# Kernel tuning notes

Hardware: AMD Instinct MI355X
Metric: run time of the kernel (lower is better)

Reference implementation:

```python
import jax, jax.numpy as jnp
import numpy as np
import math

N, E, D, H, L = 50000, 800000, 256, 8, 8
DK = D // H
DFF = 4 * D


def _layernorm(h, g, b, eps=1e-5):
    m = jnp.mean(h, axis=-1, keepdims=True)
    v = jnp.mean((h - m) ** 2, axis=-1, keepdims=True)
    return (h - m) * jax.lax.rsqrt(v + eps) * g + b


def setup_inputs() -> dict:
    key = jax.random.key(0)
    ks = jax.random.split(key, 16)
    s = 1.0 / math.sqrt(D)
    x = jax.random.normal(ks[0], (N, D), dtype=jnp.float32)
    # every node gets >=1 in-edge so z > 0 everywhere (as in real connected graphs)
    edge_src = jax.random.randint(ks[1], (E,), 0, N, dtype=jnp.int32)
    edge_dst = jnp.concatenate([
        jnp.arange(N, dtype=jnp.int32),
        jax.random.randint(ks[2], (E - N,), 0, N, dtype=jnp.int32),
    ])
    return {
        "x": x,
        "edge_src": edge_src,
        "edge_dst": edge_dst,
        "Wq": jax.random.normal(ks[3], (L, D, D), dtype=jnp.float32) * s,
        "bq": jnp.zeros((L, D), dtype=jnp.float32),
        "Wk": jax.random.normal(ks[4], (L, D, D), dtype=jnp.float32) * s,
        "Wv": jax.random.normal(ks[5], (L, D, D), dtype=jnp.float32) * s,
        "Wo": jax.random.normal(ks[6], (L, D, D), dtype=jnp.float32) * s,
        "bo": jnp.zeros((L, D), dtype=jnp.float32),
        "ln1_g": jnp.ones((L, D), dtype=jnp.float32),
        "ln1_b": jnp.zeros((L, D), dtype=jnp.float32),
        "W1": jax.random.normal(ks[7], (L, D, DFF), dtype=jnp.float32) * s,
        "b1": jnp.zeros((L, DFF), dtype=jnp.float32),
        "W2": jax.random.normal(ks[8], (L, DFF, D), dtype=jnp.float32) * (1.0 / math.sqrt(DFF)),
        "b2": jnp.zeros((L, D), dtype=jnp.float32),
        "ln2_g": jnp.ones((L, D), dtype=jnp.float32),
        "ln2_b": jnp.zeros((L, D), dtype=jnp.float32),
    }


def _layer(x, src, dst, Wq, bq, Wk, Wv, Wo, bo, g1, b1n, W1, b1, W2, b2, g2, b2n):
    n = x.shape[0]
    q = (x @ Wq + bq).reshape(n, H, DK)
    k = (x @ Wk).reshape(n, H, DK)
    v = (x @ Wv).reshape(n, H, DK)
    # edge score: src_dot_dst('k','q') -> [E, H]
    score = jnp.einsum('ehd,ehd->eh', k[src], q[dst])
    # scaled_exp: exp(clamp(score / sqrt(d_k), -5, 5))
    score = jnp.exp(jnp.clip(score / math.sqrt(DK), -5.0, 5.0))
    # u_mul_e + sum aggregation -> wv [N, H, DK]; copy_edge + sum -> z [N, H]
    msg = v[src] * score[:, :, None]
    wv = jax.ops.segment_sum(msg, dst, num_segments=n)
    z = jax.ops.segment_sum(score, dst, num_segments=n)
    o = (wv / z[:, :, None]).reshape(n, D)
    h = _layernorm(x + o @ Wo + bo, g1, b1n)
    # FFN with residual + layernorm
    ff = jax.nn.relu(h @ W1 + b1) @ W2 + b2
    return _layernorm(h + ff, g2, b2n)


def reference(x, edge_src, edge_dst, Wq, bq, Wk, Wv, Wo, bo, ln1_g, ln1_b,
              W1, b1, W2, b2, ln2_g, ln2_b):
    for i in range(L):
        x = _layer(x, edge_src, edge_dst, Wq[i], bq[i], Wk[i], Wv[i], Wo[i],
                   bo[i], ln1_g[i], ln1_b[i], W1[i], b1[i], W2[i], b2[i],
                   ln2_g[i], ln2_b[i])
    return x
```

## Files before the change

kernel.cpp:

```cpp
#include <hip/hip_runtime.h>
#include <cstdint>
#include <cstddef>

#define D 256
#define H 8
#define DFF 1024

typedef short s16x8 __attribute__((ext_vector_type(8)));
typedef float f32x4 __attribute__((ext_vector_type(4)));

static inline int cdiv(int a, int b) { return (a + b - 1) / b; }

__device__ inline uint16_t f2bf(float x) {
    unsigned u = __float_as_uint(x);
    u += 0x7FFFu + ((u >> 16) & 1u);
    return (uint16_t)(u >> 16);
}
__device__ inline float bf2f(uint16_t h) {
    return __uint_as_float(((unsigned)h) << 16);
}

__device__ inline void gload_lds16(const void* g, void* l) {
    __builtin_amdgcn_global_load_lds(
        (const __attribute__((address_space(1))) void*)g,
        (__attribute__((address_space(3))) void*)l, 16, 0, 0);
}

__device__ inline void vmcnt0() { asm volatile("s_waitcnt vmcnt(0)" ::: "memory"); }
__device__ inline void vmcnt4() { asm volatile("s_waitcnt vmcnt(4)" ::: "memory"); }
__device__ inline void vmcnt5() { asm volatile("s_waitcnt vmcnt(5)" ::: "memory"); }
__device__ inline void vmcnt6() { asm volatile("s_waitcnt vmcnt(6)" ::: "memory"); }
__device__ inline void lgkm0()  { asm volatile("s_waitcnt lgkmcnt(0)" ::: "memory"); }
#define SB0() __builtin_amdgcn_sched_barrier(0)
#define BARF() do { SB0(); __builtin_amdgcn_s_barrier(); SB0(); } while (0)

__global__ __launch_bounds__(256) void zero_int_kernel(int* __restrict__ p, int count)
{
    int i = blockIdx.x * blockDim.x + threadIdx.x;
    if (i < count) p[i] = 0;
}

__global__ __launch_bounds__(256) void count_deg_kernel(
    const int* __restrict__ edst, int* __restrict__ deg, int E)
{
    int e = blockIdx.x * blockDim.x + threadIdx.x;
    if (e < E) atomicAdd(&deg[edst[e]], 1);
}

__global__ __launch_bounds__(256) void block_sum_kernel(
    const int* __restrict__ deg, int* __restrict__ bsum, int N)
{
    int t = threadIdx.x;
    int gid = blockIdx.x * 256 + t;
    int val = (gid < N) ? deg[gid] : 0;
    #pragma unroll
    for (int o = 1; o < 64; o <<= 1) val += __shfl_xor(val, o);
    __shared__ int r[4];
    if ((t & 63) == 0) r[t >> 6] = val;
    __syncthreads();
    if (t == 0) bsum[blockIdx.x] = r[0] + r[1] + r[2] + r[3];
}

__global__ __launch_bounds__(256) void scan_bsum_kernel(int* __restrict__ bsum, int nb)
{
    __shared__ int tmp[256];
    int t = threadIdx.x;
    int val = (t < nb) ? bsum[t] : 0;
    tmp[t] = val;
    __syncthreads();
    for (int off = 1; off < 256; off <<= 1) {
        int add = (t >= off) ? tmp[t - off] : 0;
        __syncthreads();
        tmp[t] += add;
        __syncthreads();
    }
    if (t < nb) bsum[t] = tmp[t] - val;
}

__global__ __launch_bounds__(256) void scan_write_kernel(
    const int* __restrict__ deg, const int* __restrict__ bsum,
    int* __restrict__ rowptr, int* __restrict__ cursor, int N)
{
    __shared__ int tmp[256];
    int t = threadIdx.x;
    int gid = blockIdx.x * 256 + t;
    int val = (gid < N) ? deg[gid] : 0;
    tmp[t] = val;
    __syncthreads();
    for (int off = 1; off < 256; off <<= 1) {
        int add = (t >= off) ? tmp[t - off] : 0;
        __syncthreads();
        tmp[t] += add;
        __syncthreads();
    }
    int excl = tmp[t] - val + bsum[blockIdx.x];
    if (gid < N) { rowptr[gid] = excl; cursor[gid] = excl; }
    if (gid == N - 1) rowptr[N] = excl + val;
}

__global__ __launch_bounds__(256) void fill_csr_kernel(
    const int* __restrict__ esrc, const int* __restrict__ edst,
    int* __restrict__ cursor, int* __restrict__ csr_src, int E)
{
    int e = blockIdx.x * blockDim.x + threadIdx.x;
    if (e < E) {
        int pos = atomicAdd(&cursor[edst[e]], 1);
        csr_src[pos] = esrc[e];
    }
}

__global__ __launch_bounds__(256) void transpose_cast_kernel(
    const float* __restrict__ in, uint16_t* __restrict__ out,
    int R, int C, size_t inLS, size_t outLS)
{
    __shared__ float t[32][33];
    in  += blockIdx.z * inLS;
    out += blockIdx.z * outLS;
    int c0 = blockIdx.x * 32, r0 = blockIdx.y * 32;
    int tx = threadIdx.x, ty = threadIdx.y;
    #pragma unroll
    for (int i = 0; i < 4; ++i)
        t[ty + i * 8][tx] = in[(size_t)(r0 + ty + i * 8) * C + c0 + tx];
    __syncthreads();
    #pragma unroll
    for (int i = 0; i < 4; ++i)
        out[(size_t)(c0 + ty + i * 8) * R + r0 + tx] = f2bf(t[tx][ty + i * 8]);
}

__global__ __launch_bounds__(256) void cast_f32_bf16_kernel(
    const float* __restrict__ in, uint16_t* __restrict__ out, int n4)
{
    int i = blockIdx.x * blockDim.x + threadIdx.x;
    if (i >= n4) return;
    float4 f = ((const float4*)in)[i];
    uint16_t o0 = f2bf(f.x), o1 = f2bf(f.y), o2 = f2bf(f.z), o3 = f2bf(f.w);
    uint2 pk;
    pk.x = (unsigned)o0 | ((unsigned)o1 << 16);
    pk.y = (unsigned)o2 | ((unsigned)o3 << 16);
    ((uint2*)out)[i] = pk;
}

__global__ __launch_bounds__(256) void build_qkv_bias_kernel(
    const float* __restrict__ bq, float* __restrict__ qb, int total)
{
    int i = blockIdx.x * blockDim.x + threadIdx.x;
    if (i >= total) return;
    int l = i / 768, c = i - l * 768;
    qb[i] = (c < 256) ? bq[l * 256 + c] : 0.f;
}

__global__ __launch_bounds__(256) void gemm_bf16_kernel(
    const uint16_t* __restrict__ A, int lda, int M, int K,
    const uint16_t* __restrict__ BT, int Nc,
    const float* __restrict__ bias,
    uint16_t* __restrict__ Cb, int relu)
{
    __shared__ __align__(16) uint16_t As[2][128 * 32];
    __shared__ __align__(16) uint16_t Bs[2][128 * 32];

    const int tid  = threadIdx.x;
    const int lane = tid & 63;
    const int w    = tid >> 6;
    const int wr   = w >> 1, wc = w & 1;
    const int quad = lane >> 4;
    const int l15  = lane & 15;

    const int nwg = gridDim.x * gridDim.y;
    const int lin = blockIdx.y * gridDim.x + blockIdx.x;
    const int xcd = lin & 7, idx = lin >> 3;
    const int q8 = nwg >> 3, r8 = nwg & 7;
    const int lin2 = (xcd < r8 ? xcd * (q8 + 1) : r8 * (q8 + 1) + (xcd - r8) * q8) + idx;
    const int mt = lin2 % gridDim.x;
    const int nt = lin2 / gridDim.x;

    const int m0 = mt * 128;
    const int n0 = nt * 128;

    f32x4 acc[4][4] = {};

    const int jbase = w * 2;
    const int srow  = lane >> 2;
    const int skc   = (lane & 3) * 8;

    auto stage = [&](int b, int k0) {
        #pragma unroll
        for (int jj = 0; jj < 2; ++jj) {
            int j = jbase + jj;
            int r = j * 16 + srow;
            int gr = m0 + r; if (gr > M - 1) gr = M - 1;
            gload_lds16(A  + (size_t)gr * lda + k0 + skc, &As[b][j * 512]);
            gload_lds16(BT + (size_t)(n0 + r) * K + k0 + skc, &Bs[b][j * 512]);
        }
    };

    const int nsteps = K >> 5;
    stage(0, 0);
    for (int s = 0; s < nsteps; ++s) {
        if (s + 1 < nsteps) { stage((s + 1) & 1, (s + 1) << 5); vmcnt4(); }
        else vmcnt0();
        BARF();
        const int b = s & 1;
        s16x8 af[4], bf[4];
        #pragma unroll
        for (int t = 0; t < 4; ++t) {
            af[t] = *(const s16x8*)&As[b][(wr * 64 + t * 16 + l15) * 32 + quad * 8];
            bf[t] = *(const s16x8*)&Bs[b][(wc * 64 + t * 16 + l15) * 32 + quad * 8];
        }
        #pragma unroll
        for (int i = 0; i < 4; ++i)
            #pragma unroll
            for (int jt = 0; jt < 4; ++jt)
                acc[i][jt] = __builtin_amdgcn_mfma_f32_16x16x32_bf16(
                    af[i], bf[jt], acc[i][jt], 0, 0, 0);
        BARF();
    }

    float bv[4];
    #pragma unroll
    for (int jt = 0; jt < 4; ++jt)
        bv[jt] = bias ? bias[n0 + wc * 64 + jt * 16 + l15] : 0.f;

    #pragma unroll
    for (int i = 0; i < 4; ++i) {
        #pragma unroll
        for (int r = 0; r < 4; ++r) {
            int m = m0 + wr * 64 + i * 16 + quad * 4 + r;
            if (m >= M) continue;
            #pragma unroll
            for (int jt = 0; jt < 4; ++jt) {
                int n = n0 + wc * 64 + jt * 16 + l15;
                float val = acc[i][jt][r] + bv[jt];
                if (relu) val = fmaxf(val, 0.f);
                Cb[(size_t)m * Nc + n] = f2bf(val);
            }
        }
    }
}

__global__ __launch_bounds__(256) void gemm_ln_kernel(
    const uint16_t* __restrict__ A, int lda, int M, int K,
    const uint16_t* __restrict__ BT,
    const float* __restrict__ bias,
    const float* __restrict__ resid,
    const float* __restrict__ g, const float* __restrict__ b,
    float* __restrict__ Cf, uint16_t* __restrict__ Cb)
{
    __shared__ __align__(16) uint16_t As[2][64 * 32];
    __shared__ __align__(16) uint16_t Bs[2][256 * 32];
    __shared__ float sS[64][4];
    __shared__ float sQ[64][4];

    const int tid  = threadIdx.x;
    const int lane = tid & 63;
    const int w    = tid >> 6;
    const int quad = lane >> 4;
    const int l15  = lane & 15;

    const int m0 = blockIdx.x * 64;

    f32x4 acc[4][4] = {};

    auto stage = [&](int bb, int k0) {
        {
            int r = tid >> 2, kc = (tid & 3) * 8;
            int gr = m0 + r; if (gr > M - 1) gr = M - 1;
            gload_lds16(A + (size_t)gr * lda + k0 + kc, &As[bb][tid * 8]);
        }
        #pragma unroll
        for (int i = 0; i < 4; ++i) {
            int slot = i * 256 + tid;
            int n = slot >> 2, kc = (slot & 3) * 8;
            gload_lds16(BT + (size_t)n * K + k0 + kc, &Bs[bb][slot * 8]);
        }
    };

    const int nsteps = K >> 5;
    stage(0, 0);
    for (int s = 0; s < nsteps; ++s) {
        if (s + 1 < nsteps) { stage((s + 1) & 1, (s + 1) << 5); vmcnt5(); }
        else vmcnt0();
        BARF();
        const int bb = s & 1;
        s16x8 af[4], bf[4];
        #pragma unroll
        for (int t = 0; t < 4; ++t) {
            af[t] = *(const s16x8*)&As[bb][(t * 16 + l15) * 32 + quad * 8];
            bf[t] = *(const s16x8*)&Bs[bb][(w * 64 + t * 16 + l15) * 32 + quad * 8];
        }
        #pragma unroll
        for (int i = 0; i < 4; ++i)
            #pragma unroll
            for (int jt = 0; jt < 4; ++jt)
                acc[i][jt] = __builtin_amdgcn_mfma_f32_16x16x32_bf16(
                    af[i], bf[jt], acc[i][jt], 0, 0, 0);
        BARF();
    }

    float bv[4], gv[4], bbv[4];
    #pragma unroll
    for (int jt = 0; jt < 4; ++jt) {
        int n = w * 64 + jt * 16 + l15;
        bv[jt]  = bias[n];
        gv[jt]  = g[n];
        bbv[jt] = b[n];
    }

    #pragma unroll
    for (int i = 0; i < 4; ++i) {
        #pragma unroll
        for (int r = 0; r < 4; ++r) {
            int ml = i * 16 + quad * 4 + r;
            int m  = m0 + ml;
            bool valid = (m < M);
            float s = 0.f, s2 = 0.f;
            #pragma unroll
            for (int jt = 0; jt < 4; ++jt) {
                int n = w * 64 + jt * 16 + l15;
                float val = acc[i][jt][r] + bv[jt];
                if (valid) val += resid[(size_t)m * 256 + n];
                acc[i][jt][r] = val;
                s += val;
                s2 += val * val;
            }
            #pragma unroll
            for (int o = 1; o < 16; o <<= 1) {
                s  += __shfl_xor(s, o);
                s2 += __shfl_xor(s2, o);
            }
            if (l15 == 0) { sS[ml][w] = s; sQ[ml][w] = s2; }
        }
    }
    __syncthreads();

    #pragma unroll
    for (int i = 0; i < 4; ++i) {
        #pragma unroll
        for (int r = 0; r < 4; ++r) {
            int ml = i * 16 + quad * 4 + r;
            int m  = m0 + ml;
            if (m >= M) continue;
            float s  = sS[ml][0] + sS[ml][1] + sS[ml][2] + sS[ml][3];
            float s2 = sQ[ml][0] + sQ[ml][1] + sQ[ml][2] + sQ[ml][3];
            float mean = s * (1.f / 256.f);
            float var  = s2 * (1.f / 256.f) - mean * mean;
            float rstd = rsqrtf(var + 1e-5f);
            #pragma unroll
            for (int jt = 0; jt < 4; ++jt) {
                int n = w * 64 + jt * 16 + l15;
                float out = (acc[i][jt][r] - mean) * rstd * gv[jt] + bbv[jt];
                Cf[(size_t)m * 256 + n] = out;
                if (Cb) Cb[(size_t)m * 256 + n] = f2bf(out);
            }
        }
    }
}

__global__ __launch_bounds__(256) void ffn_fused_kernel(
    const uint16_t* __restrict__ A,
    int M,
    const uint16_t* __restrict__ BT1,
    const float* __restrict__ b1,
    const uint16_t* __restrict__ BT2,
    const float* __restrict__ b2,
    const float* __restrict__ resid,
    const float* __restrict__ g, const float* __restrict__ b,
    float* __restrict__ Cf, uint16_t* __restrict__ Cb)
{
    __shared__ __align__(16) uint16_t U[3][8192];
    __shared__ __align__(16) uint16_t Ts[4][64][32];

    const int tid  = threadIdx.x;
    const int lane = tid & 63;
    const int w    = tid >> 6;
    const int quad = lane >> 4;
    const int l15  = lane & 15;
    const int m0   = blockIdx.x * 64;

    f32x4 acc2[4][4] = {};

    auto issue = [&](int q) {
        if (q >= 96) return;
        const int slot = q % 3;
        const int qc = q / 12;
        const int r  = q - qc * 12;
        if (r < 8) {
            const int k0 = r << 5;
            {
                int rr = tid >> 2, kc = (tid & 3) * 8;
                int gr = m0 + rr; if (gr > M - 1) gr = M - 1;
                gload_lds16(A + (size_t)gr * 256 + k0 + kc, &U[slot][tid * 8]);
            }
            #pragma unroll
            for (int i = 0; i < 2; ++i) {
                int s2 = i * 256 + tid;
                int n = s2 >> 2, kc = (s2 & 3) * 8;
                gload_lds16(BT1 + (size_t)(qc * 128 + n) * 256 + k0 + kc,
                            &U[slot][2048 + s2 * 8]);
            }
        } else {
            const int ts = r - 8;
            #pragma unroll
            for (int i = 0; i < 4; ++i) {
                int s2 = i * 256 + tid;
                int n = s2 >> 2, kc = (s2 & 3) * 8;
                gload_lds16(BT2 + (size_t)n * 1024 + qc * 128 + ts * 32 + kc,
                            &U[slot][s2 * 8]);
            }
        }
    };

    issue(0);
    issue(1);

    for (int c = 0; c < 8; ++c) {
        f32x4 acc1[4][2] = {};
        const int pbase = c * 12;

        for (int ks = 0; ks < 8; ++ks) {
            const int p = pbase + ks;
            issue(p + 2);
            vmcnt6();
            BARF();
            const uint16_t* Us = U[p % 3];
            s16x8 af[4], bf1[2];
            #pragma unroll
            for (int t = 0; t < 4; ++t)
                af[t] = *(const s16x8*)&Us[(t * 16 + l15) * 32 + quad * 8];
            #pragma unroll
            for (int jt = 0; jt < 2; ++jt)
                bf1[jt] = *(const s16x8*)&Us[2048 + (w * 32 + jt * 16 + l15) * 32 + quad * 8];
            #pragma unroll
            for (int i = 0; i < 4; ++i)
                #pragma unroll
                for (int jt = 0; jt < 2; ++jt)
                    acc1[i][jt] = __builtin_amdgcn_mfma_f32_16x16x32_bf16(
                        af[i], bf1[jt], acc1[i][jt], 0, 0, 0);
            BARF();
        }

        float bv1[2];
        #pragma unroll
        for (int jt = 0; jt < 2; ++jt)
            bv1[jt] = b1[c * 128 + w * 32 + jt * 16 + l15];
        {
            uint16_t* tsw = &Ts[w][0][0];
            #pragma unroll
            for (int i = 0; i < 4; ++i)
                #pragma unroll
                for (int r = 0; r < 4; ++r) {
                    int ml = i * 16 + quad * 4 + r;
                    int sw = ((ml >> 1) & 3) << 3;
                    #pragma unroll
                    for (int jt = 0; jt < 2; ++jt) {
                        float val = acc1[i][jt][r] + bv1[jt];
                        val = fmaxf(val, 0.f);
                        tsw[(ml * 32 + jt * 16 + l15) ^ sw] = f2bf(val);
                    }
                }
        }
        lgkm0();
        BARF();

        for (int ts = 0; ts < 4; ++ts) {
            const int p = pbase + 8 + ts;
            issue(p + 2);
            if (c == 7 && ts == 2) vmcnt4();
            else if (c == 7 && ts == 3) vmcnt0();
            else vmcnt6();
            BARF();
            const uint16_t* Us = U[p % 3];
            const uint16_t* tsr = &Ts[ts][0][0];
            s16x8 af2[4], bf2[4];
            #pragma unroll
            for (int i = 0; i < 4; ++i) {
                int row = i * 16 + l15;
                af2[i] = *(const s16x8*)&tsr[(row * 32 + quad * 8) ^ (((row >> 1) & 3) << 3)];
            }
            #pragma unroll
            for (int jt = 0; jt < 4; ++jt)
                bf2[jt] = *(const s16x8*)&Us[(w * 64 + jt * 16 + l15) * 32 + quad * 8];
            #pragma unroll
            for (int i = 0; i < 4; ++i)
                #pragma unroll
                for (int jt = 0; jt < 4; ++jt)
                    acc2[i][jt] = __builtin_amdgcn_mfma_f32_16x16x32_bf16(
                        af2[i], bf2[jt], acc2[i][jt], 0, 0, 0);
            BARF();
        }
    }

    float* sS = (float*)&U[0][0];
    float* sQ = (float*)&U[0][512];

    float bv[4], gv[4], bbv[4];
    #pragma unroll
    for (int jt = 0; jt < 4; ++jt) {
        int n = w * 64 + jt * 16 + l15;
        bv[jt]  = b2[n];
        gv[jt]  = g[n];
        bbv[jt] = b[n];
    }

    #pragma unroll
    for (int i = 0; i < 4; ++i) {
        #pragma unroll
        for (int r = 0; r < 4; ++r) {
            int ml = i * 16 + quad * 4 + r;
            int m  = m0 + ml;
            bool valid = (m < M);
            float s = 0.f, s2 = 0.f;
            #pragma unroll
            for (int jt = 0; jt < 4; ++jt) {
                float val = acc2[i][jt][r] + bv[jt];
                if (valid) val += resid[(size_t)m * 256 + w * 64 + jt * 16 + l15];
                acc2[i][jt][r] = val;
                s += val;
                s2 += val * val;
            }
            #pragma unroll
            for (int o = 1; o < 16; o <<= 1) {
                s  += __shfl_xor(s, o);
                s2 += __shfl_xor(s2, o);
            }
            if (l15 == 0) { sS[ml * 4 + w] = s; sQ[ml * 4 + w] = s2; }
        }
    }
    __syncthreads();

    #pragma unroll
    for (int i = 0; i < 4; ++i) {
        #pragma unroll
        for (int r = 0; r < 4; ++r) {
            int ml = i * 16 + quad * 4 + r;
            int m  = m0 + ml;
            if (m >= M) continue;
            float s  = sS[ml * 4 + 0] + sS[ml * 4 + 1] + sS[ml * 4 + 2] + sS[ml * 4 + 3];
            float s2 = sQ[ml * 4 + 0] + sQ[ml * 4 + 1] + sQ[ml * 4 + 2] + sQ[ml * 4 + 3];
            float mean = s * (1.f / 256.f);
            float var  = s2 * (1.f / 256.f) - mean * mean;
            float rstd = rsqrtf(var + 1e-5f);
            #pragma unroll
            for (int jt = 0; jt < 4; ++jt) {
                int n = w * 64 + jt * 16 + l15;
                float out = (acc2[i][jt][r] - mean) * rstd * gv[jt] + bbv[jt];
                Cf[(size_t)m * 256 + n] = out;
                if (Cb) Cb[(size_t)m * 256 + n] = f2bf(out);
            }
        }
    }
}

__global__ __launch_bounds__(256) void node_attn_kernel(
    uint16_t* __restrict__ qkv,
    const int* __restrict__ rowptr, const int* __restrict__ csr_src, int N)
{
    int node = (blockIdx.x * blockDim.x + threadIdx.x) >> 6;
    int lane = threadIdx.x & 63;
    if (node >= N) return;

    uint16_t* qp = qkv + (size_t)node * 768 + lane * 4;
    uint2 qu = *(const uint2*)qp;
    float q0 = bf2f((uint16_t)(qu.x & 0xFFFF)), q1 = bf2f((uint16_t)(qu.x >> 16));
    float q2 = bf2f((uint16_t)(qu.y & 0xFFFF)), q3 = bf2f((uint16_t)(qu.y >> 16));

    float a0 = 0.f, a1 = 0.f, a2 = 0.f, a3 = 0.f, zacc = 0.f;
    const float inv_sqrt_dk = 0.17677669529663687f;

    int beg = rowptr[node], end = rowptr[node + 1];
    int i = beg;
    for (; i + 1 < end; i += 2) {
        int s0 = csr_src[i], s1 = csr_src[i + 1];
        const uint16_t* b0 = qkv + (size_t)s0 * 768;
        const uint16_t* b1 = qkv + (size_t)s1 * 768;
        uint2 ku0 = *(const uint2*)(b0 + 256 + lane * 4);
        uint2 ku1 = *(const uint2*)(b1 + 256 + lane * 4);
        uint2 vu0 = *(const uint2*)(b0 + 512 + lane * 4);
        uint2 vu1 = *(const uint2*)(b1 + 512 + lane * 4);

        float p0 = bf2f((uint16_t)(ku0.x & 0xFFFF)) * q0
                 + bf2f((uint16_t)(ku0.x >> 16))   * q1
                 + bf2f((uint16_t)(ku0.y & 0xFFFF)) * q2
                 + bf2f((uint16_t)(ku0.y >> 16))   * q3;
        float p1 = bf2f((uint16_t)(ku1.x & 0xFFFF)) * q0
                 + bf2f((uint16_t)(ku1.x >> 16))   * q1
                 + bf2f((uint16_t)(ku1.y & 0xFFFF)) * q2
                 + bf2f((uint16_t)(ku1.y >> 16))   * q3;
        p0 += __shfl_xor(p0, 1); p1 += __shfl_xor(p1, 1);
        p0 += __shfl_xor(p0, 2); p1 += __shfl_xor(p1, 2);
        p0 += __shfl_xor(p0, 4); p1 += __shfl_xor(p1, 4);
        float sc0 = __expf(fminf(fmaxf(p0 * inv_sqrt_dk, -5.f), 5.f));
        float sc1 = __expf(fminf(fmaxf(p1 * inv_sqrt_dk, -5.f), 5.f));

        a0 += bf2f((uint16_t)(vu0.x & 0xFFFF)) * sc0;
        a1 += bf2f((uint16_t)(vu0.x >> 16))   * sc0;
        a2 += bf2f((uint16_t)(vu0.y & 0xFFFF)) * sc0;
        a3 += bf2f((uint16_t)(vu0.y >> 16))   * sc0;
        zacc += sc0;
        a0 += bf2f((uint16_t)(vu1.x & 0xFFFF)) * sc1;
        a1 += bf2f((uint16_t)(vu1.x >> 16))   * sc1;
        a2 += bf2f((uint16_t)(vu1.y & 0xFFFF)) * sc1;
        a3 += bf2f((uint16_t)(vu1.y >> 16))   * sc1;
        zacc += sc1;
    }
    if (i < end) {
        int s = csr_src[i];
        const uint16_t* base = qkv + (size_t)s * 768;
        uint2 ku = *(const uint2*)(base + 256 + lane * 4);
        float p = bf2f((uint16_t)(ku.x & 0xFFFF)) * q0
                + bf2f((uint16_t)(ku.x >> 16))   * q1
                + bf2f((uint16_t)(ku.y & 0xFFFF)) * q2
                + bf2f((uint16_t)(ku.y >> 16))   * q3;
        p += __shfl_xor(p, 1);
        p += __shfl_xor(p, 2);
        p += __shfl_xor(p, 4);
        float sc = __expf(fminf(fmaxf(p * inv_sqrt_dk, -5.f), 5.f));
        uint2 vu = *(const uint2*)(base + 512 + lane * 4);
        a0 += bf2f((uint16_t)(vu.x & 0xFFFF)) * sc;
        a1 += bf2f((uint16_t)(vu.x >> 16))   * sc;
        a2 += bf2f((uint16_t)(vu.y & 0xFFFF)) * sc;
        a3 += bf2f((uint16_t)(vu.y >> 16))   * sc;
        zacc += sc;
    }
    float inv = 1.f / zacc;
    uint2 pk;
    pk.x = (unsigned)f2bf(a0 * inv) | ((unsigned)f2bf(a1 * inv) << 16);
    pk.y = (unsigned)f2bf(a2 * inv) | ((unsigned)f2bf(a3 * inv) << 16);
    *(uint2*)qp = pk;
}

extern "C" void kernel_launch(void* const* d_in, const int* in_sizes, int n_in,
                              void* d_out, int out_size, void* d_ws, size_t ws_size,
                              hipStream_t stream)
{
    const float* x0   = (const float*)d_in[0];
    const int* esrc   = (const int*)d_in[1];
    const int* edst   = (const int*)d_in[2];
    const float* Wq   = (const float*)d_in[3];
    const float* bq   = (const float*)d_in[4];
    const float* Wk   = (const float*)d_in[5];
    const float* Wv   = (const float*)d_in[6];
    const float* Wo   = (const float*)d_in[7];
    const float* bo   = (const float*)d_in[8];
    const float* ln1g = (const float*)d_in[9];
    const float* ln1b = (const float*)d_in[10];
    const float* W1   = (const float*)d_in[11];
    const float* b1   = (const float*)d_in[12];
    const float* W2   = (const float*)d_in[13];
    const float* b2   = (const float*)d_in[14];
    const float* ln2g = (const float*)d_in[15];
    const float* ln2b = (const float*)d_in[16];

    const int N = in_sizes[0] / D;
    const int E = in_sizes[1];
    const int L = in_sizes[3] / (D * D);
    const size_t ND = (size_t)N * D;

    char* p = (char*)d_ws;
    float* bufX = (float*)p;         p += ND * 4;
    uint16_t* xb  = (uint16_t*)p;    p += ND * 2;
    uint16_t* qkv = (uint16_t*)p;    p += (size_t)N * 768 * 2;
    uint16_t* hb  = (uint16_t*)p;    p += ND * 2;
    uint16_t* BTqkv = (uint16_t*)p;  p += (size_t)L * 768 * 256 * 2;
    uint16_t* BTo   = (uint16_t*)p;  p += (size_t)L * 256 * 256 * 2;
    uint16_t* BT1   = (uint16_t*)p;  p += (size_t)L * 1024 * 256 * 2;
    uint16_t* BT2   = (uint16_t*)p;  p += (size_t)L * 256 * 1024 * 2;
    float* qbias    = (float*)p;     p += (size_t)L * 768 * 4;
    int* rowptr  = (int*)p;          p += (size_t)(N + 1) * 4;
    int* cursor  = (int*)p;          p += (size_t)N * 4;
    int* deg     = cursor;
    int* csr_src = (int*)p;          p += (size_t)E * 4;
    int* bsum    = (int*)p;

    const int nb = cdiv(N, 256);
    dim3 blk(256);
    int edgeBlocks = cdiv(E, 256);
    int nodeBlocks = cdiv(N, 4);

    dim3 tb(32, 8);
    transpose_cast_kernel<<<dim3(8, 8, L), tb, 0, stream>>>(Wq, BTqkv, 256, 256, (size_t)65536, (size_t)768 * 256);
    transpose_cast_kernel<<<dim3(8, 8, L), tb, 0, stream>>>(Wk, BTqkv + 256 * 256, 256, 256, (size_t)65536, (size_t)768 * 256);
    transpose_cast_kernel<<<dim3(8, 8, L), tb, 0, stream>>>(Wv, BTqkv + 512 * 256, 256, 256, (size_t)65536, (size_t)768 * 256);
    transpose_cast_kernel<<<dim3(8, 8, L), tb, 0, stream>>>(Wo, BTo, 256, 256, (size_t)65536, (size_t)65536);
    transpose_cast_kernel<<<dim3(32, 8, L), tb, 0, stream>>>(W1, BT1, 256, 1024, (size_t)262144, (size_t)262144);
    transpose_cast_kernel<<<dim3(8, 32, L), tb, 0, stream>>>(W2, BT2, 1024, 256, (size_t)262144, (size_t)262144);
    build_qkv_bias_kernel<<<cdiv(L * 768, 256), blk, 0, stream>>>(bq, qbias, L * 768);
    cast_f32_bf16_kernel<<<cdiv((int)(ND / 4), 256), blk, 0, stream>>>(x0, xb, (int)(ND / 4));

    zero_int_kernel<<<cdiv(N, 256), blk, 0, stream>>>(deg, N);
    count_deg_kernel<<<edgeBlocks, blk, 0, stream>>>(edst, deg, E);
    block_sum_kernel<<<nb, blk, 0, stream>>>(deg, bsum, N);
    scan_bsum_kernel<<<1, blk, 0, stream>>>(bsum, nb);
    scan_write_kernel<<<nb, blk, 0, stream>>>(deg, bsum, rowptr, cursor, N);
    fill_csr_kernel<<<edgeBlocks, blk, 0, stream>>>(esrc, edst, cursor, csr_src, E);

    const int Mt128 = cdiv(N, 128);
    const int Mt64  = cdiv(N, 64);
    dim3 gQKV(Mt128, 768 / 128);
    dim3 gLN(Mt64, 1);

    for (int l = 0; l < L; ++l) {
        const uint16_t* BTqkv_l = BTqkv + (size_t)l * 768 * 256;
        const uint16_t* BTo_l   = BTo + (size_t)l * 65536;
        const uint16_t* BT1_l   = BT1 + (size_t)l * 262144;
        const uint16_t* BT2_l   = BT2 + (size_t)l * 262144;
        const float* xin_f = (l == 0) ? x0 : bufX;

        gemm_bf16_kernel<<<gQKV, blk, 0, stream>>>(xb, 256, N, 256, BTqkv_l, 768,
            qbias + (size_t)l * 768, qkv, 0);

        node_attn_kernel<<<nodeBlocks, blk, 0, stream>>>(qkv, rowptr, csr_src, N);

        gemm_ln_kernel<<<gLN, blk, 0, stream>>>(qkv, 768, N, 256, BTo_l,
            bo + (size_t)l * 256, xin_f, ln1g + (size_t)l * 256, ln1b + (size_t)l * 256,
            bufX, hb);

        float* fout = (l == L - 1) ? (float*)d_out : bufX;
        ffn_fused_kernel<<<gLN, blk, 0, stream>>>(hb, N, BT1_l,
            b1 + (size_t)l * 1024, BT2_l, b2 + (size_t)l * 256, bufX,
            ln2g + (size_t)l * 256, ln2b + (size_t)l * 256,
            fout, (l == L - 1) ? nullptr : xb);

        xin_f = bufX;
    }
}
```

Before: 3.901 ms.

## Enlarge fused FFN tile to 128 rows with shared hidden buffer and double-buffering

The fused FFN kernel now handles 128 rows per block instead of 64. Each weight tile loaded into LDS is therefore reused across twice as many rows, which halves the W1/W2 global traffic per row. The intermediate ReLU tile moves into one padded 128x144 shared array (no XOR swizzle), and the triple-buffered prefetch becomes double-buffered with prefetch distance one. In exchange the block uses twice the accumulator registers, which can lower occupancy. The grid is also halved, and the shallower prefetch may expose more load latency.

Result: faster. 3.519 ms (-9.8%).

```diff
diff --git a/kernel.cpp b/kernel.cpp
--- a/kernel.cpp
+++ b/kernel.cpp
@@ -29,7 +29,6 @@
 __device__ inline void vmcnt0() { asm volatile("s_waitcnt vmcnt(0)" ::: "memory"); }
 __device__ inline void vmcnt4() { asm volatile("s_waitcnt vmcnt(4)" ::: "memory"); }
 __device__ inline void vmcnt5() { asm volatile("s_waitcnt vmcnt(5)" ::: "memory"); }
-__device__ inline void vmcnt6() { asm volatile("s_waitcnt vmcnt(6)" ::: "memory"); }
 __device__ inline void lgkm0()  { asm volatile("s_waitcnt lgkmcnt(0)" ::: "memory"); }
 #define SB0() __builtin_amdgcn_sched_barrier(0)
 #define BARF() do { SB0(); __builtin_amdgcn_s_barrier(); SB0(); } while (0)
@@ -366,95 +365,92 @@
     const float* __restrict__ g, const float* __restrict__ b,
     float* __restrict__ Cf, uint16_t* __restrict__ Cb)
 {
-    __shared__ __align__(16) uint16_t U[3][8192];
-    __shared__ __align__(16) uint16_t Ts[4][64][32];
+    __shared__ __align__(16) uint16_t U[2][8192];
+    __shared__ __align__(16) uint16_t Ts[128][144];
 
     const int tid  = threadIdx.x;
     const int lane = tid & 63;
     const int w    = tid >> 6;
     const int quad = lane >> 4;
     const int l15  = lane & 15;
-    const int m0   = blockIdx.x * 64;
-
-    f32x4 acc2[4][4] = {};
+    const int m0   = blockIdx.x * 128;
+
+    f32x4 acc2[8][4] = {};
 
     auto issue = [&](int q) {
         if (q >= 96) return;
-        const int slot = q % 3;
-        const int qc = q / 12;
-        const int r  = q - qc * 12;
+        const int slot = q & 1;
+        const int c = q / 12;
+        const int r = q - c * 12;
+        const int row = tid >> 2, kc = (tid & 3) * 8;
         if (r < 8) {
             const int k0 = r << 5;
-            {
-                int rr = tid >> 2, kc = (tid & 3) * 8;
+            #pragma unroll
+            for (int i = 0; i < 2; ++i) {
+                int rr = row + i * 64;
                 int gr = m0 + rr; if (gr > M - 1) gr = M - 1;
-                gload_lds16(A + (size_t)gr * 256 + k0 + kc, &U[slot][tid * 8]);
+                gload_lds16(A + (size_t)gr * 256 + k0 + kc,
+                            &U[slot][(i * 256 + tid) * 8]);
             }
             #pragma unroll
             for (int i = 0; i < 2; ++i) {
-                int s2 = i * 256 + tid;
-                int n = s2 >> 2, kc = (s2 & 3) * 8;
-                gload_lds16(BT1 + (size_t)(qc * 128 + n) * 256 + k0 + kc,
-                            &U[slot][2048 + s2 * 8]);
+                int rr = row + i * 64;
+                gload_lds16(BT1 + (size_t)(c * 128 + rr) * 256 + k0 + kc,
+                            &U[slot][4096 + (i * 256 + tid) * 8]);
             }
         } else {
             const int ts = r - 8;
             #pragma unroll
             for (int i = 0; i < 4; ++i) {
-                int s2 = i * 256 + tid;
-                int n = s2 >> 2, kc = (s2 & 3) * 8;
-                gload_lds16(BT2 + (size_t)n * 1024 + qc * 128 + ts * 32 + kc,
-                            &U[slot][s2 * 8]);
+                int rr = row + i * 64;
+                gload_lds16(BT2 + (size_t)rr * 1024 + c * 128 + ts * 32 + kc,
+                            &U[slot][(i * 256 + tid) * 8]);
             }
         }
     };
 
     issue(0);
-    issue(1);
 
     for (int c = 0; c < 8; ++c) {
-        f32x4 acc1[4][2] = {};
-        const int pbase = c * 12;
+        f32x4 acc1[8][2] = {};
+        const int pb = c * 12;
 
         for (int ks = 0; ks < 8; ++ks) {
-            const int p = pbase + ks;
-            issue(p + 2);
-            vmcnt6();
+            const int p = pb + ks;
+            issue(p + 1);
+            vmcnt4();
             BARF();
-            const uint16_t* Us = U[p % 3];
-            s16x8 af[4], bf1[2];
-            #pragma unroll
-            for (int t = 0; t < 4; ++t)
-                af[t] = *(const s16x8*)&Us[(t * 16 + l15) * 32 + quad * 8];
+            const uint16_t* Us = U[p & 1];
+            s16x8 bf1[2];
             #pragma unroll
             for (int jt = 0; jt < 2; ++jt)
-                bf1[jt] = *(const s16x8*)&Us[2048 + (w * 32 + jt * 16 + l15) * 32 + quad * 8];
-            #pragma unroll
-            for (int i = 0; i < 4; ++i)
-                #pragma unroll
-                for (int jt = 0; jt < 2; ++jt)
-                    acc1[i][jt] = __builtin_amdgcn_mfma_f32_16x16x32_bf16(
-                        af[i], bf1[jt], acc1[i][jt], 0, 0, 0);
+                bf1[jt] = *(const s16x8*)&Us[4096 + (w * 32 + jt * 16 + l15) * 32 + quad * 8];
+            #pragma unroll
+            for (int i = 0; i < 8; ++i) {
+                s16x8 af = *(const s16x8*)&Us[(i * 16 + l15) * 32 + quad * 8];
+                acc1[i][0] = __builtin_amdgcn_mfma_f32_16x16x32_bf16(
+                    af, bf1[0], acc1[i][0], 0, 0, 0);
+                acc1[i][1] = __builtin_amdgcn_mfma_f32_16x16x32_bf16(
+                    af, bf1[1], acc1[i][1], 0, 0, 0);
+            }
             BARF();
         }
 
-        float bv1[2];
-        #pragma unroll
-        for (int jt = 0; jt < 2; ++jt)
-            bv1[jt] = b1[c * 128 + w * 32 + jt * 16 + l15];
         {
-            uint16_t* tsw = &Ts[w][0][0];
-            #pragma unroll
-            for (int i = 0; i < 4; ++i)
+            float bv1[2];
+            #pragma unroll
+            for (int jt = 0; jt < 2; ++jt)
+                bv1[jt] = b1[c * 128 + w * 32 + jt * 16 + l15];
+            #pragma unroll
+            for (int i = 0; i < 8; ++i)
                 #pragma unroll
                 for (int r = 0; r < 4; ++r) {
                     int ml = i * 16 + quad * 4 + r;
-                    int sw = ((ml >> 1) & 3) << 3;
                     #pragma unroll
                     for (int jt = 0; jt < 2; ++jt) {
                         float val = acc1[i][jt][r] + bv1[jt];
                         val = fmaxf(val, 0.f);
-                        tsw[(ml * 32 + jt * 16 + l15) ^ sw] = f2bf(val);
+                        Ts[ml][w * 32 + jt * 16 + l15] = f2bf(val);
                     }
                 }
         }
@@ -462,35 +458,29 @@
         BARF();
 
         for (int ts = 0; ts < 4; ++ts) {
-            const int p = pbase + 8 + ts;
-            issue(p + 2);
-            if (c == 7 && ts == 2) vmcnt4();
-            else if (c == 7 && ts == 3) vmcnt0();
-            else vmcnt6();
+            const int p = pb + 8 + ts;
+            issue(p + 1);
+            if (p == 95) vmcnt0(); else vmcnt4();
             BARF();
-            const uint16_t* Us = U[p % 3];
-            const uint16_t* tsr = &Ts[ts][0][0];
-            s16x8 af2[4], bf2[4];
-            #pragma unroll
-            for (int i = 0; i < 4; ++i) {
-                int row = i * 16 + l15;
-                af2[i] = *(const s16x8*)&tsr[(row * 32 + quad * 8) ^ (((row >> 1) & 3) << 3)];
-            }
+            const uint16_t* Us = U[p & 1];
+            s16x8 bf2[4];
             #pragma unroll
             for (int jt = 0; jt < 4; ++jt)
                 bf2[jt] = *(const s16x8*)&Us[(w * 64 + jt * 16 + l15) * 32 + quad * 8];
             #pragma unroll
-            for (int i = 0; i < 4; ++i)
+            for (int i = 0; i < 8; ++i) {
+                s16x8 af2 = *(const s16x8*)&Ts[i * 16 + l15][ts * 32 + quad * 8];
                 #pragma unroll
                 for (int jt = 0; jt < 4; ++jt)
                     acc2[i][jt] = __builtin_amdgcn_mfma_f32_16x16x32_bf16(
-                        af2[i], bf2[jt], acc2[i][jt], 0, 0, 0);
+                        af2, bf2[jt], acc2[i][jt], 0, 0, 0);
+            }
             BARF();
         }
     }
 
     float* sS = (float*)&U[0][0];
-    float* sQ = (float*)&U[0][512];
+    float* sQ = (float*)&U[0][1024];
 
     float bv[4], gv[4], bbv[4];
     #pragma unroll
@@ -502,7 +492,7 @@
     }
 
     #pragma unroll
-    for (int i = 0; i < 4; ++i) {
+    for (int i = 0; i < 8; ++i) {
         #pragma unroll
         for (int r = 0; r < 4; ++r) {
             int ml = i * 16 + quad * 4 + r;
@@ -528,7 +518,7 @@
     __syncthreads();
 
     #pragma unroll
-    for (int i = 0; i < 4; ++i) {
+    for (int i = 0; i < 8; ++i) {
         #pragma unroll
         for (int r = 0; r < 4; ++r) {
             int ml = i * 16 + quad * 4 + r;
@@ -697,6 +687,7 @@
     const int Mt64  = cdiv(N, 64);
     dim3 gQKV(Mt128, 768 / 128);
     dim3 gLN(Mt64, 1);
+    dim3 gFFN(Mt128, 1);
 
     for (int l = 0; l < L; ++l) {
         const uint16_t* BTqkv_l = BTqkv + (size_t)l * 768 * 256;
@@ -715,7 +706,7 @@
             bufX, hb);
 
         float* fout = (l == L - 1) ? (float*)d_out : bufX;
-        ffn_fused_kernel<<<gLN, blk, 0, stream>>>(hb, N, BT1_l,
+        ffn_fused_kernel<<<gFFN, blk, 0, stream>>>(hb, N, BT1_l,
             b1 + (size_t)l * 1024, BT2_l, b2 + (size_t)l * 256, bufX,
             ln2g + (size_t)l * 256, ln2b + (size_t)l * 256,
             fout, (l == L - 1) ? nullptr : xb);
```
